# Optimization experiments

Hardware: AMD Instinct MI355X
Metric: run time of the kernel (lower is better)

The kernel has to match this reference:

```python
import jax, jax.numpy as jnp
import numpy as np

B, S, D = 4, 8192, 1024   # batch, seq_len, d_model
DG = 256                  # genre embedding dim
E, K = 64, 2              # n_experts, top_k


def setup_inputs() -> dict:
    key = jax.random.key(0)
    k1, k2, k3, k4 = jax.random.split(key, 4)
    x = jax.random.normal(k1, (B, S, D), dtype=jnp.float32)
    genre_emb = jax.random.normal(k2, (B, DG), dtype=jnp.float32)
    # router parameters (kaiming-ish scale)
    Wx = jax.random.normal(k3, (D, E), dtype=jnp.float32) / np.sqrt(D)
    Wg = jax.random.normal(k4, (DG, E), dtype=jnp.float32) / np.sqrt(DG)
    b = jnp.zeros((E,), dtype=jnp.float32)
    return {"x": x, "genre_emb": genre_emb, "Wx": Wx, "Wg": Wg, "b": b}


def reference(x, genre_emb, Wx, Wg, b):
    # Router logits conditioned on token state and broadcast genre embedding.
    # x: [B,S,D], genre_emb: [B,DG] -> logits [B,S,E]
    logits = jnp.einsum("bsd,de->bse", x, Wx) + (genre_emb @ Wg)[:, None, :] + b
    probs = jax.nn.softmax(logits, axis=-1)          # [B,S,E]
    topk_vals, topk_idx = jax.lax.top_k(probs, K)    # [B,S,K]
    # renormalize selected expert weights to sum to 1
    topk_vals = topk_vals / topk_vals.sum(axis=-1, keepdims=True)
    # scatter back to sparse dense gate tensor [B,S,E]
    onehot = jax.nn.one_hot(topk_idx, E, dtype=topk_vals.dtype)  # [B,S,K,E]
    gates = jnp.einsum("bsk,bske->bse", topk_vals, onehot)
    return gates, topk_idx
```

## Files before the change

kernel.cpp:

```cpp
#include <hip/hip_runtime.h>
#include <math.h>

#define NTOK   32768
#define DMODEL 1024
#define NEXP   64
#define DGENRE 256
#define BK     64
#define TT     64

typedef const __attribute__((address_space(1))) void ga_void;
typedef __attribute__((address_space(3))) void lds_void;

__device__ __forceinline__ bool better(float va, int ia, float vb, int ib) {
  return (va > vb) || (va == vb && ia < ib);
}

__global__ __launch_bounds__(256, 4) void moe_gate_k(
    const float* __restrict__ x, const float* __restrict__ Wx,
    const float* __restrict__ genre, const float* __restrict__ Wg,
    const float* __restrict__ bias, float* __restrict__ out) {
  __shared__ __align__(16) float xs[2][TT * BK];
  __shared__ float cpart[4][NEXP];
  __shared__ float cbias[NEXP];

  const int tid  = threadIdx.x;
  const int wv   = tid >> 6;
  const int lane = tid & 63;
  const int tok0 = blockIdx.x * TT;
  const int b    = tok0 >> 13;

  {
    const int e = tid & 63, dc = tid >> 6;
    const float* g  = genre + b * DGENRE + dc * 64;
    const float* wg = Wg + (size_t)(dc * 64) * NEXP + e;
    float p = 0.f;
#pragma unroll 8
    for (int d = 0; d < 64; ++d) p = fmaf(g[d], wg[(size_t)d * NEXP], p);
    cpart[dc][e] = p;
  }

  const int eg = tid & 15;
  const int tg = tid >> 4;
  const int e0 = eg * 4;
  const int t0 = tg * 4;
  const int sw = tg & 3;

  float acc[4][4] = {{0.f}};

#define STAGE(bufidx, d0)                                                      \
  {                                                                            \
    _Pragma("unroll")                                                          \
    for (int s = 0; s < 4; ++s) {                                              \
      const int L = wv * 256 + s * 64 + lane;                                  \
      const int t = L >> 4, pq = L & 15;                                       \
      const int dq = pq ^ ((t >> 2) & 3);                                      \
      const float* gsrc = x + (size_t)(tok0 + t) * DMODEL + (d0) + dq * 4;     \
      __builtin_amdgcn_global_load_lds((ga_void*)gsrc,                         \
          (lds_void*)&xs[bufidx][L * 4], 16, 0, 0);                            \
    }                                                                          \
  }

#define COMPUTE(bufidx, d0)                                                    \
  {                                                                            \
    const float* xb = &xs[bufidx][0];                                          \
    const float* wp = Wx + (size_t)(d0) * NEXP + e0;                           \
    _Pragma("unroll 2")                                                        \
    for (int dq = 0; dq < 16; ++dq) {                                          \
      float4 xv[4], wv4[4];                                                    \
      _Pragma("unroll")                                                        \
      for (int i = 0; i < 4; ++i)                                              \
        xv[i] = *reinterpret_cast<const float4*>(                              \
            &xb[(t0 + i) * BK + ((dq ^ sw) << 2)]);                            \
      _Pragma("unroll")                                                        \
      for (int dd = 0; dd < 4; ++dd)                                           \
        wv4[dd] = *reinterpret_cast<const float4*>(                            \
            &wp[(size_t)(dq * 4 + dd) * NEXP]);                                \
      _Pragma("unroll")                                                        \
      for (int dd = 0; dd < 4; ++dd) {                                         \
        _Pragma("unroll")                                                      \
        for (int i = 0; i < 4; ++i) {                                          \
          const float xvv = reinterpret_cast<const float*>(&xv[i])[dd];        \
          _Pragma("unroll")                                                    \
          for (int j = 0; j < 4; ++j)                                          \
            acc[i][j] = fmaf(                                                  \
                xvv, reinterpret_cast<const float*>(&wv4[dd])[j], acc[i][j]);  \
        }                                                                      \
      }                                                                        \
    }                                                                          \
  }

  STAGE(0, 0);
  __syncthreads();
  if (tid < NEXP)
    cbias[tid] = bias[tid] + cpart[0][tid] + cpart[1][tid] + cpart[2][tid] +
                 cpart[3][tid];

  for (int c = 0; c < DMODEL / BK; ++c) {
    if (c < DMODEL / BK - 1) STAGE((c + 1) & 1, (c + 1) * BK);
    COMPUTE(c & 1, c * BK);
    __syncthreads();
  }

#pragma unroll
  for (int j = 0; j < 4; ++j) {
    const float cb = cbias[e0 + j];
#pragma unroll
    for (int i = 0; i < 4; ++i) acc[i][j] += cb;
  }

  float* gates  = out;
  float* idxout = out + (size_t)NTOK * NEXP;

#pragma unroll
  for (int i = 0; i < 4; ++i) {
    float v1 = acc[i][0]; int i1 = e0;
    float v2 = -INFINITY; int i2 = NEXP;
#pragma unroll
    for (int j = 1; j < 4; ++j) {
      const float a = acc[i][j]; const int ei = e0 + j;
      if (better(a, ei, v1, i1)) { v2 = v1; i2 = i1; v1 = a; i1 = ei; }
      else if (better(a, ei, v2, i2)) { v2 = a; i2 = ei; }
    }
#pragma unroll
    for (int m = 1; m < 16; m <<= 1) {
      const float ov1 = __shfl_xor(v1, m, 64); const int oi1 = __shfl_xor(i1, m, 64);
      const float ov2 = __shfl_xor(v2, m, 64); const int oi2 = __shfl_xor(i2, m, 64);
      if (better(v1, i1, ov1, oi1)) {
        if (better(ov1, oi1, v2, i2)) { v2 = ov1; i2 = oi1; }
      } else {
        if (better(v1, i1, ov2, oi2)) { v2 = v1; i2 = i1; }
        else                          { v2 = ov2; i2 = oi2; }
        v1 = ov1; i1 = oi1;
      }
    }
    const float ew  = expf(v2 - v1);
    const float inv = 1.0f / (1.0f + ew);
    const float w1 = inv, w2 = ew * inv;

    const int tok = tok0 + t0 + i;
    float4 g;
    g.x = (e0 + 0 == i1) ? w1 : ((e0 + 0 == i2) ? w2 : 0.0f);
    g.y = (e0 + 1 == i1) ? w1 : ((e0 + 1 == i2) ? w2 : 0.0f);
    g.z = (e0 + 2 == i1) ? w1 : ((e0 + 2 == i2) ? w2 : 0.0f);
    g.w = (e0 + 3 == i1) ? w1 : ((e0 + 3 == i2) ? w2 : 0.0f);
    *reinterpret_cast<float4*>(&gates[(size_t)tok * NEXP + e0]) = g;

    if (eg == 0) {
      idxout[(size_t)tok * 2 + 0] = (float)i1;
      idxout[(size_t)tok * 2 + 1] = (float)i2;
    }
  }
}

extern "C" void kernel_launch(void* const* d_in, const int* in_sizes, int n_in,
                              void* d_out, int out_size, void* d_ws, size_t ws_size,
                              hipStream_t stream) {
  const float* x     = (const float*)d_in[0];
  const float* genre = (const float*)d_in[1];
  const float* Wx    = (const float*)d_in[2];
  const float* Wg    = (const float*)d_in[3];
  const float* bias  = (const float*)d_in[4];
  float* out = (float*)d_out;

  moe_gate_k<<<NTOK / TT, 256, 0, stream>>>(x, Wx, genre, Wg, bias, out);
}
```

Measured before the change: 274.5 us.

## Assign one token per lane with wave-split K and LDS reduction

Changes the work split so each lane owns one token and accumulates all 64 experts in registers. Each of the four waves handles a quarter of every BK chunk, and partial sums are combined through LDS at the end. Wx rows are read as wave-uniform loads (wv made uniform via readfirstlane), so they can become scalar loads broadcast to all lanes, removing per-thread vector loads of Wx and the cross-lane shuffle top-k. The trade-offs are 64 accumulator registers per thread, which may lower occupancy, an extra LDS reduction phase, and a serial per-lane top-2 scan with uncoalesced per-token gate stores.

```diff
diff --git a/kernel.cpp b/kernel.cpp
--- a/kernel.cpp
+++ b/kernel.cpp
@@ -7,25 +7,22 @@
 #define DGENRE 256
 #define BK     64
 #define TT     64
+#define NCHUNK (DMODEL / BK)
 
 typedef const __attribute__((address_space(1))) void ga_void;
 typedef __attribute__((address_space(3))) void lds_void;
-
-__device__ __forceinline__ bool better(float va, int ia, float vb, int ib) {
-  return (va > vb) || (va == vb && ia < ib);
-}
 
 __global__ __launch_bounds__(256, 4) void moe_gate_k(
     const float* __restrict__ x, const float* __restrict__ Wx,
     const float* __restrict__ genre, const float* __restrict__ Wg,
     const float* __restrict__ bias, float* __restrict__ out) {
-  __shared__ __align__(16) float xs[2][TT * BK];
+  __shared__ __align__(16) float smem[2 * TT * BK];
   __shared__ float cpart[4][NEXP];
   __shared__ float cbias[NEXP];
 
   const int tid  = threadIdx.x;
-  const int wv   = tid >> 6;
   const int lane = tid & 63;
+  const int wv   = __builtin_amdgcn_readfirstlane(tid >> 6);
   const int tok0 = blockIdx.x * TT;
   const int b    = tok0 >> 13;
 
@@ -39,52 +36,41 @@
     cpart[dc][e] = p;
   }
 
-  const int eg = tid & 15;
-  const int tg = tid >> 4;
-  const int e0 = eg * 4;
-  const int t0 = tg * 4;
-  const int sw = tg & 3;
-
-  float acc[4][4] = {{0.f}};
+  float acc[NEXP];
+#pragma unroll
+  for (int e = 0; e < NEXP; ++e) acc[e] = 0.f;
 
 #define STAGE(bufidx, d0)                                                      \
   {                                                                            \
     _Pragma("unroll")                                                          \
     for (int s = 0; s < 4; ++s) {                                              \
-      const int L = wv * 256 + s * 64 + lane;                                  \
-      const int t = L >> 4, pq = L & 15;                                       \
-      const int dq = pq ^ ((t >> 2) & 3);                                      \
+      const int SL = s * 256 + tid;                                            \
+      const int t  = SL >> 4;                                                  \
+      const int q  = SL & 15;                                                  \
+      const int dq = q ^ (t & 7);                                              \
       const float* gsrc = x + (size_t)(tok0 + t) * DMODEL + (d0) + dq * 4;     \
       __builtin_amdgcn_global_load_lds((ga_void*)gsrc,                         \
-          (lds_void*)&xs[bufidx][L * 4], 16, 0, 0);                            \
+          (lds_void*)&smem[(bufidx) * 4096 + (s * 256 + wv * 64) * 4],         \
+          16, 0, 0);                                                           \
     }                                                                          \
   }
 
-#define COMPUTE(bufidx, d0)                                                    \
+#define COMPUTE(bufidx, c)                                                     \
   {                                                                            \
-    const float* xb = &xs[bufidx][0];                                          \
-    const float* wp = Wx + (size_t)(d0) * NEXP + e0;                           \
-    _Pragma("unroll 2")                                                        \
-    for (int dq = 0; dq < 16; ++dq) {                                          \
-      float4 xv[4], wv4[4];                                                    \
-      _Pragma("unroll")                                                        \
-      for (int i = 0; i < 4; ++i)                                              \
-        xv[i] = *reinterpret_cast<const float4*>(                              \
-            &xb[(t0 + i) * BK + ((dq ^ sw) << 2)]);                            \
-      _Pragma("unroll")                                                        \
-      for (int dd = 0; dd < 4; ++dd)                                           \
-        wv4[dd] = *reinterpret_cast<const float4*>(                            \
-            &wp[(size_t)(dq * 4 + dd) * NEXP]);                                \
+    _Pragma("unroll")                                                          \
+    for (int r = 0; r < 4; ++r) {                                              \
+      const float4 xq4 = *reinterpret_cast<const float4*>(                     \
+          &smem[(bufidx) * 4096 + lane * BK +                                  \
+                (((wv * 4 + r) ^ (lane & 7)) << 2)]);                          \
+      const float* xa = reinterpret_cast<const float*>(&xq4);                  \
       _Pragma("unroll")                                                        \
       for (int dd = 0; dd < 4; ++dd) {                                         \
+        const float* wrow =                                                    \
+            Wx + (size_t)((c) * BK + wv * 16 + r * 4 + dd) * NEXP;             \
+        const float xd = xa[dd];                                               \
         _Pragma("unroll")                                                      \
-        for (int i = 0; i < 4; ++i) {                                          \
-          const float xvv = reinterpret_cast<const float*>(&xv[i])[dd];        \
-          _Pragma("unroll")                                                    \
-          for (int j = 0; j < 4; ++j)                                          \
-            acc[i][j] = fmaf(                                                  \
-                xvv, reinterpret_cast<const float*>(&wv4[dd])[j], acc[i][j]);  \
-        }                                                                      \
+        for (int e = 0; e < NEXP; ++e)                                         \
+          acc[e] = fmaf(xd, wrow[e], acc[e]);                                  \
       }                                                                        \
     }                                                                          \
   }
@@ -95,60 +81,68 @@
     cbias[tid] = bias[tid] + cpart[0][tid] + cpart[1][tid] + cpart[2][tid] +
                  cpart[3][tid];
 
-  for (int c = 0; c < DMODEL / BK; ++c) {
-    if (c < DMODEL / BK - 1) STAGE((c + 1) & 1, (c + 1) * BK);
-    COMPUTE(c & 1, c * BK);
+  for (int c = 0; c < NCHUNK; ++c) {
+    if (c < NCHUNK - 1) STAGE((c + 1) & 1, (c + 1) * BK);
+    COMPUTE(c & 1, c);
     __syncthreads();
   }
 
+  if (wv >= 2) {
+    const int base = (wv - 2) * 4096;
 #pragma unroll
-  for (int j = 0; j < 4; ++j) {
-    const float cb = cbias[e0 + j];
+    for (int e = 0; e < NEXP; ++e) smem[base + e * 64 + lane] = acc[e];
+  }
+  __syncthreads();
+  if (wv < 2) {
+    const int base = wv * 4096;
 #pragma unroll
-    for (int i = 0; i < 4; ++i) acc[i][j] += cb;
+    for (int e = 0; e < NEXP; ++e) acc[e] += smem[base + e * 64 + lane];
   }
+  __syncthreads();
+  if (wv == 1) {
+#pragma unroll
+    for (int e = 0; e < NEXP; ++e) smem[e * 64 + lane] = acc[e];
+  }
+  __syncthreads();
 
-  float* gates  = out;
-  float* idxout = out + (size_t)NTOK * NEXP;
+  if (wv == 0) {
+#pragma unroll
+    for (int e = 0; e < NEXP; ++e) acc[e] += smem[e * 64 + lane] + cbias[e];
 
-#pragma unroll
-  for (int i = 0; i < 4; ++i) {
-    float v1 = acc[i][0]; int i1 = e0;
+    float v1 = acc[0]; int i1 = 0;
     float v2 = -INFINITY; int i2 = NEXP;
 #pragma unroll
-    for (int j = 1; j < 4; ++j) {
-      const float a = acc[i][j]; const int ei = e0 + j;
-      if (better(a, ei, v1, i1)) { v2 = v1; i2 = i1; v1 = a; i1 = ei; }
-      else if (better(a, ei, v2, i2)) { v2 = a; i2 = ei; }
+    for (int e = 1; e < NEXP; ++e) {
+      const float a  = acc[e];
+      const bool g1 = a > v1;
+      const bool g2 = a > v2;
+      const float nv2 = g1 ? v1 : (g2 ? a : v2);
+      const int   ni2 = g1 ? i1 : (g2 ? e : i2);
+      v1 = g1 ? a : v1;
+      i1 = g1 ? e : i1;
+      v2 = nv2;
+      i2 = ni2;
     }
-#pragma unroll
-    for (int m = 1; m < 16; m <<= 1) {
-      const float ov1 = __shfl_xor(v1, m, 64); const int oi1 = __shfl_xor(i1, m, 64);
-      const float ov2 = __shfl_xor(v2, m, 64); const int oi2 = __shfl_xor(i2, m, 64);
-      if (better(v1, i1, ov1, oi1)) {
-        if (better(ov1, oi1, v2, i2)) { v2 = ov1; i2 = oi1; }
-      } else {
-        if (better(v1, i1, ov2, oi2)) { v2 = v1; i2 = i1; }
-        else                          { v2 = ov2; i2 = oi2; }
-        v1 = ov1; i1 = oi1;
-      }
-    }
+
     const float ew  = expf(v2 - v1);
     const float inv = 1.0f / (1.0f + ew);
     const float w1 = inv, w2 = ew * inv;
 
-    const int tok = tok0 + t0 + i;
-    float4 g;
-    g.x = (e0 + 0 == i1) ? w1 : ((e0 + 0 == i2) ? w2 : 0.0f);
-    g.y = (e0 + 1 == i1) ? w1 : ((e0 + 1 == i2) ? w2 : 0.0f);
-    g.z = (e0 + 2 == i1) ? w1 : ((e0 + 2 == i2) ? w2 : 0.0f);
-    g.w = (e0 + 3 == i1) ? w1 : ((e0 + 3 == i2) ? w2 : 0.0f);
-    *reinterpret_cast<float4*>(&gates[(size_t)tok * NEXP + e0]) = g;
-
-    if (eg == 0) {
-      idxout[(size_t)tok * 2 + 0] = (float)i1;
-      idxout[(size_t)tok * 2 + 1] = (float)i2;
+    float* gates = out + (size_t)(tok0 + lane) * NEXP;
+#pragma unroll
+    for (int eq = 0; eq < 16; ++eq) {
+      float4 g;
+      float* gp = reinterpret_cast<float*>(&g);
+#pragma unroll
+      for (int k = 0; k < 4; ++k) {
+        const int e = eq * 4 + k;
+        gp[k] = (e == i1) ? w1 : ((e == i2) ? w2 : 0.0f);
+      }
+      *reinterpret_cast<float4*>(&gates[eq * 4]) = g;
     }
+    float* idxout = out + (size_t)NTOK * NEXP + (size_t)(tok0 + lane) * 2;
+    idxout[0] = (float)i1;
+    idxout[1] = (float)i2;
   }
 }
 
```

Measured after the change: 372.9 us. 35.8% more time.
